# Performance work log

Hardware: AMD Instinct MI355X
Metric: run time of the kernel (lower is better)

The kernel has to match this reference:

```python
import jax, jax.numpy as jnp
import numpy as np

B, NQ, NK, D, H, DFF = 4, 1024, 1024, 1024, 16, 4096
DH = D // H
SCALE = 1.0 / np.sqrt(D).astype(np.float32)  # torch code scales by sqrt(dim_V), not head_dim
LN_EPS = 1e-5


def setup_inputs() -> dict:
    key = jax.random.key(0)
    ks = jax.random.split(key, 20)
    s = lambda fan_in: 1.0 / np.sqrt(fan_in).astype(np.float32)
    inp = {
        "Q": jax.random.normal(ks[0], (B, NQ, D), jnp.float32),
        "K": jax.random.normal(ks[1], (B, NK, D), jnp.float32),
        # attention projections (torch Linear stored here as [in, out])
        "Wq": jax.random.uniform(ks[2], (D, D), jnp.float32, -s(D), s(D)),
        "bq": jnp.zeros((D,), jnp.float32),
        "Wk": jax.random.uniform(ks[3], (D, D), jnp.float32, -s(D), s(D)),
        "bk": jnp.zeros((D,), jnp.float32),
        "Wv": jax.random.uniform(ks[4], (D, D), jnp.float32, -s(D), s(D)),
        "bv": jnp.zeros((D,), jnp.float32),
        "Wo": jax.random.uniform(ks[5], (D, D), jnp.float32, -s(D), s(D)),
        "bo": jnp.zeros((D,), jnp.float32),
        # FFN
        "W1": jax.random.uniform(ks[6], (D, DFF), jnp.float32, -s(D), s(D)),
        "b1": jnp.zeros((DFF,), jnp.float32),
        "W2": jax.random.uniform(ks[7], (DFF, D), jnp.float32, -s(DFF), s(DFF)),
        "b2": jnp.zeros((D,), jnp.float32),
        # LayerNorms
        "g0": jnp.ones((D,), jnp.float32),
        "be0": jnp.zeros((D,), jnp.float32),
        "g1": jnp.ones((D,), jnp.float32),
        "be1": jnp.zeros((D,), jnp.float32),
    }
    return inp


def _layernorm(x, g, b):
    mu = x.mean(-1, keepdims=True)
    var = ((x - mu) ** 2).mean(-1, keepdims=True)
    return (x - mu) * jax.lax.rsqrt(var + LN_EPS) * g + b


def reference(Q, K, Wq, bq, Wk, bk, Wv, bv, Wo, bo, W1, b1, W2, b2, g0, be0, g1, be1):
    # multi-head attention (MHA path, mask=None)
    q = (Q @ Wq + bq).reshape(B, NQ, H, DH)
    k = (K @ Wk + bk).reshape(B, NK, H, DH)
    v = (K @ Wv + bv).reshape(B, NK, H, DH)
    E = jnp.einsum("bqhd,bkhd->bhqk", q, k) * SCALE  # [B,H,NQ,NK]
    A = jax.nn.softmax(E, axis=-1)
    O = jnp.einsum("bhqk,bkhd->bqhd", A, v).reshape(B, NQ, D)
    O = O @ Wo + bo
    # residual + LN0
    X = _layernorm(Q + O, g0, be0)
    # FFN + residual + LN1
    Y = jnp.maximum(X @ W1 + b1, 0.0) @ W2 + b2
    return _layernorm(X + Y, g1, be1)
```

## Files before the change

kernel.cpp:

```cpp
#include <hip/hip_runtime.h>
#include <math.h>

#define B_   4
#define NQ_  1024
#define NK_  1024
#define D_   1024
#define H_   16
#define DH_  64
#define DFF_ 4096
#define SCALE_ (1.0f/32.0f)
#define LN_EPS_ 1e-5f

typedef __attribute__((ext_vector_type(8))) short bf16x8_t;
typedef __attribute__((ext_vector_type(4))) float f32x4_t;

__device__ __forceinline__ ushort f2bf_rne(float x) {
    unsigned u = __float_as_uint(x);
    unsigned r = (u + 0x7FFFu + ((u >> 16) & 1u)) >> 16;
    return (ushort)r;
}
__device__ __forceinline__ float bf2f(ushort h) {
    return __uint_as_float(((unsigned)h) << 16);
}

__device__ __forceinline__ void gl_lds16(const ushort* g, ushort* l) {
    __builtin_amdgcn_global_load_lds(
        (const __attribute__((address_space(1))) unsigned int*)g,
        (__attribute__((address_space(3))) unsigned int*)l, 16, 0, 0);
}

__global__ __launch_bounds__(256) void split_rows(const float* __restrict__ src,
        ushort* __restrict__ hi, ushort* __restrict__ lo, int n4)
{
    int i = blockIdx.x * 256 + threadIdx.x;
    if (i >= n4) return;
    float4 v = ((const float4*)src)[i];
    ushort4 h, l;
    h.x = f2bf_rne(v.x); l.x = f2bf_rne(v.x - bf2f(h.x));
    h.y = f2bf_rne(v.y); l.y = f2bf_rne(v.y - bf2f(h.y));
    h.z = f2bf_rne(v.z); l.z = f2bf_rne(v.z - bf2f(h.z));
    h.w = f2bf_rne(v.w); l.w = f2bf_rne(v.w - bf2f(h.w));
    ((ushort4*)hi)[i] = h;
    ((ushort4*)lo)[i] = l;
}

__global__ __launch_bounds__(256) void split_tr(const float* __restrict__ Wsrc,
        ushort* __restrict__ th, ushort* __restrict__ tl, int K, int N)
{
    __shared__ float tile[32][33];
    const int nb = blockIdx.x * 32, kb = blockIdx.y * 32;
    const int t = threadIdx.x;
    {
        int r = t >> 3, c4 = (t & 7) * 4;
        float4 v = *(const float4*)&Wsrc[(size_t)(kb + r) * N + nb + c4];
        tile[r][c4 + 0] = v.x; tile[r][c4 + 1] = v.y;
        tile[r][c4 + 2] = v.z; tile[r][c4 + 3] = v.w;
    }
    __syncthreads();
    {
        int n = t >> 3, k4 = (t & 7) * 4;
        float a0 = tile[k4 + 0][n], a1 = tile[k4 + 1][n];
        float a2 = tile[k4 + 2][n], a3 = tile[k4 + 3][n];
        ushort4 h, l;
        h.x = f2bf_rne(a0); l.x = f2bf_rne(a0 - bf2f(h.x));
        h.y = f2bf_rne(a1); l.y = f2bf_rne(a1 - bf2f(h.y));
        h.z = f2bf_rne(a2); l.z = f2bf_rne(a2 - bf2f(h.z));
        h.w = f2bf_rne(a3); l.w = f2bf_rne(a3 - bf2f(h.w));
        size_t o = (size_t)(nb + n) * K + kb + k4;
        *(ushort4*)&th[o] = h;
        *(ushort4*)&tl[o] = l;
    }
}

template<bool RELU, int OMODE>
__device__ __forceinline__ void gemm_body(
        const ushort* __restrict__ Ah, const ushort* __restrict__ Al,
        const ushort* __restrict__ Bh, const ushort* __restrict__ Bl,
        const float* __restrict__ bias,
        float* __restrict__ C, ushort* __restrict__ Ch, ushort* __restrict__ Cl,
        int M, int N, int Kd, int Klen, int brow, int bcol)
{
    __shared__ __align__(16) ushort S[2][4][128 * 32];

    const int t    = threadIdx.x;
    const int lane = t & 63;
    const int w    = t >> 6;
    const int wr   = (w >> 1) * 64;
    const int wc   = (w & 1) * 64;
    const int fr   = lane & 15;
    const int g    = lane >> 4;
    const int sS   = ((g ^ ((fr >> 1) & 3)) << 3);
    const int cl   = lane & 15;
    const int rq   = (lane >> 4) * 4;

    float bpre[4];
    #pragma unroll
    for (int j = 0; j < 4; ++j)
        bpre[j] = bias ? bias[bcol + wc + j * 16 + cl] : 0.f;

    f32x4_t acc[4][4];
    #pragma unroll
    for (int i = 0; i < 4; ++i)
        #pragma unroll
        for (int j = 0; j < 4; ++j)
            acc[i][j] = (f32x4_t){0.f, 0.f, 0.f, 0.f};

    const int lrow  = lane >> 2;
    const int lslot = ((lane & 3) ^ ((lane >> 3) & 3)) << 3;
    const int c0    = w * 2;

    auto issue2 = [&](const ushort* gpp, int rb, int pl, int buf, int k0) {
        #pragma unroll
        for (int ii = 0; ii < 2; ++ii) {
            int c = c0 + ii;
            gl_lds16(gpp + (size_t)(rb + c * 16 + lrow) * Kd + k0 + lslot,
                     &S[buf][pl][c * 512]);
        }
    };

    bf16x8_t ahf[4], bhf[4], blf[4], alf[4];

    issue2(Ah, brow, 0, 0, 0);
    issue2(Bh, bcol, 2, 0, 0);
    issue2(Bl, bcol, 3, 0, 0);
    issue2(Al, brow, 1, 0, 0);
    asm volatile("s_waitcnt vmcnt(4)" ::: "memory");
    __builtin_amdgcn_s_barrier();

    const int NT = Klen >> 5;
    for (int tt = 0; tt < NT; ++tt) {
        const int cur = tt & 1, nxt = cur ^ 1;
        const int kn  = (tt + 1) << 5;
        const bool more = (tt + 1 < NT);

        #pragma unroll
        for (int i = 0; i < 4; ++i)
            ahf[i] = *(const bf16x8_t*)&S[cur][0][(wr + i * 16 + fr) * 32 + sS];
        #pragma unroll
        for (int j = 0; j < 4; ++j)
            bhf[j] = *(const bf16x8_t*)&S[cur][2][(wc + j * 16 + fr) * 32 + sS];
        if (more) {
            issue2(Ah, brow, 0, nxt, kn);
            issue2(Bh, bcol, 2, nxt, kn);
            asm volatile("s_waitcnt vmcnt(6)" ::: "memory");
        } else {
            asm volatile("s_waitcnt vmcnt(2)" ::: "memory");
        }
        __builtin_amdgcn_s_barrier();
        asm volatile("s_waitcnt lgkmcnt(0)" ::: "memory");
        __builtin_amdgcn_sched_barrier(0);
        __builtin_amdgcn_s_setprio(1);
        #pragma unroll
        for (int i = 0; i < 4; ++i)
            #pragma unroll
            for (int j = 0; j < 4; ++j)
                acc[i][j] = __builtin_amdgcn_mfma_f32_16x16x32_bf16(ahf[i], bhf[j], acc[i][j], 0, 0, 0);
        __builtin_amdgcn_s_setprio(0);
        __builtin_amdgcn_s_barrier();

        #pragma unroll
        for (int j = 0; j < 4; ++j)
            blf[j] = *(const bf16x8_t*)&S[cur][3][(wc + j * 16 + fr) * 32 + sS];
        if (more) {
            issue2(Bl, bcol, 3, nxt, kn);
            asm volatile("s_waitcnt vmcnt(6)" ::: "memory");
        } else {
            asm volatile("s_waitcnt vmcnt(0)" ::: "memory");
        }
        __builtin_amdgcn_s_barrier();
        asm volatile("s_waitcnt lgkmcnt(0)" ::: "memory");
        __builtin_amdgcn_sched_barrier(0);
        __builtin_amdgcn_s_setprio(1);
        #pragma unroll
        for (int i = 0; i < 4; ++i)
            #pragma unroll
            for (int j = 0; j < 4; ++j)
                acc[i][j] = __builtin_amdgcn_mfma_f32_16x16x32_bf16(ahf[i], blf[j], acc[i][j], 0, 0, 0);
        __builtin_amdgcn_s_setprio(0);
        __builtin_amdgcn_s_barrier();

        #pragma unroll
        for (int i = 0; i < 4; ++i)
            alf[i] = *(const bf16x8_t*)&S[cur][1][(wr + i * 16 + fr) * 32 + sS];
        if (more) {
            issue2(Al, brow, 1, nxt, kn);
            asm volatile("s_waitcnt vmcnt(4)" ::: "memory");
        }
        __builtin_amdgcn_s_barrier();
        asm volatile("s_waitcnt lgkmcnt(0)" ::: "memory");
        __builtin_amdgcn_sched_barrier(0);
        __builtin_amdgcn_s_setprio(1);
        #pragma unroll
        for (int i = 0; i < 4; ++i)
            #pragma unroll
            for (int j = 0; j < 4; ++j)
                acc[i][j] = __builtin_amdgcn_mfma_f32_16x16x32_bf16(alf[i], bhf[j], acc[i][j], 0, 0, 0);
        __builtin_amdgcn_s_setprio(0);
        __builtin_amdgcn_s_barrier();
    }

    if (OMODE == 0) {
        #pragma unroll
        for (int j = 0; j < 4; ++j) {
            int col = bcol + wc + j * 16 + cl;
            #pragma unroll
            for (int i = 0; i < 4; ++i)
                #pragma unroll
                for (int r = 0; r < 4; ++r) {
                    int row = brow + wr + i * 16 + rq + r;
                    float v = acc[i][j][r] + bpre[j];
                    if (RELU) v = fmaxf(v, 0.f);
                    C[(size_t)row * N + col] = v;
                }
        }
    } else {
        float* E = (float*)&S[0][0][0] + w * 4096;
        #pragma unroll
        for (int j = 0; j < 4; ++j) {
            #pragma unroll
            for (int i = 0; i < 4; ++i)
                #pragma unroll
                for (int r = 0; r < 4; ++r) {
                    float v = acc[i][j][r] + bpre[j];
                    if (RELU) v = fmaxf(v, 0.f);
                    E[(i * 16 + rq + r) * 64 + j * 16 + cl] = v;
                }
        }
        __syncthreads();
        const int rr8 = lane >> 3;
        const int c8  = (lane & 7) * 8;
        #pragma unroll
        for (int p = 0; p < 8; ++p) {
            int rl = p * 8 + rr8;
            float4 va = *(float4*)&E[rl * 64 + c8];
            float4 vb = *(float4*)&E[rl * 64 + c8 + 4];
            float v[8] = {va.x, va.y, va.z, va.w, vb.x, vb.y, vb.z, vb.w};
            bf16x8_t hv, lv;
            #pragma unroll
            for (int q = 0; q < 8; ++q) {
                ushort hh = f2bf_rne(v[q]);
                hv[q] = (short)hh;
                lv[q] = (short)f2bf_rne(v[q] - bf2f(hh));
            }
            size_t o = (size_t)(brow + wr + rl) * N + (bcol + wc + c8);
            *(bf16x8_t*)&Ch[o] = hv;
            if (OMODE == 1) *(bf16x8_t*)&Cl[o] = lv;
        }
    }
}

__device__ __forceinline__ void swz_block(int& brow, int& bcol, int tile) {
    const int nx  = gridDim.x;
    const int lin = blockIdx.y * nx + blockIdx.x;
    const int cpx = (nx * gridDim.y) >> 3;
    const int swz = (lin & 7) * cpx + (lin >> 3);
    brow = (swz / nx) * tile;
    bcol = (swz % nx) * tile;
}

template<bool RELU, int OMODE>
__global__ __launch_bounds__(256) void gemm_mfma(
        const ushort* __restrict__ Ah, const ushort* __restrict__ Al,
        const ushort* __restrict__ Bh, const ushort* __restrict__ Bl,
        const float* __restrict__ bias,
        float* __restrict__ C, ushort* __restrict__ Ch, ushort* __restrict__ Cl,
        int M, int N, int Kd)
{
    int brow, bcol;
    swz_block(brow, bcol, 128);
    gemm_body<RELU, OMODE>(Ah, Al, Bh, Bl, bias, C, Ch, Cl, M, N, Kd, Kd, brow, bcol);
}

__global__ __launch_bounds__(256) void gemm_splitk2(
        const ushort* __restrict__ Ah, const ushort* __restrict__ Al,
        const ushort* __restrict__ Bh, const ushort* __restrict__ Bl,
        const float* __restrict__ bias,
        float* __restrict__ C0, float* __restrict__ C1,
        int M, int N, int Kd)
{
    int brow, bcol;
    swz_block(brow, bcol, 128);
    const int z = blockIdx.z;
    const int Kh2 = Kd >> 1;
    const int ko  = z * Kh2;
    gemm_body<false, 0>(Ah + ko, Al + ko, Bh + ko, Bl + ko,
                        z == 0 ? bias : nullptr,
                        z == 0 ? C0 : C1, nullptr, nullptr,
                        M, N, Kd, Kh2, brow, bcol);
}

struct QkvArgs {
    const ushort* Ah[3]; const ushort* Al[3];
    const ushort* Bh[3]; const ushort* Bl[3];
    const float*  bias[3];
    ushort*       Co[3];
};

__global__ __launch_bounds__(256) void gemm_qkv(QkvArgs qa, int M, int N, int Kd)
{
    int brow, bcol;
    swz_block(brow, bcol, 128);
    const int z = blockIdx.z;
    gemm_body<false, 2>(qa.Ah[z], qa.Al[z], qa.Bh[z], qa.Bl[z], qa.bias[z],
                        nullptr, qa.Co[z], nullptr, M, N, Kd, Kd, brow, bcol);
}

__global__ __launch_bounds__(256) void flash_attn_mfma(
        const ushort* __restrict__ qh, const ushort* __restrict__ kh,
        const ushort* __restrict__ vh,
        ushort* __restrict__ Oh, ushort* __restrict__ Ol)
{
    __shared__ __align__(16) ushort SMEM[8192];
    ushort* sk  = SMEM;
    ushort* svt = SMEM + 2304;
    ushort* pw0 = SMEM + 4864;

    const int bid  = blockIdx.x;
    const int slot = bid >> 3;
    const int bh   = (bid & 7) * 8 + (slot >> 4);
    const int qt   = slot & 15;
    const int b    = bh >> 4;
    const int h    = bh & 15;
    const int qb   = qt * 64;

    const int t = threadIdx.x, lane = t & 63, w = t >> 6;
    const int l15 = lane & 15, g = lane >> 4;

    bf16x8_t qf[2];
    {
        size_t qrow = ((size_t)(b * NQ_) + qb + w * 16 + l15) * D_ + h * DH_;
        qf[0] = *(const bf16x8_t*)&qh[qrow + 0  + 8 * g];
        qf[1] = *(const bf16x8_t*)&qh[qrow + 32 + 8 * g];
    }

    f32x4_t acc[4];
    #pragma unroll
    for (int dt = 0; dt < 4; ++dt) acc[dt] = (f32x4_t){0.f, 0.f, 0.f, 0.f};
    float m = -INFINITY, l = 0.0f;

    const int kkv = t >> 3,  kds = (t & 7) * 8;
    const int vkv = t & 31,  vds = (t >> 5) * 8;
    const size_t kvbase = (size_t)(b * NK_) * D_ + h * DH_;

    bf16x8_t kreg = *(const bf16x8_t*)&kh[kvbase + (size_t)kkv * D_ + kds];
    bf16x8_t vreg = *(const bf16x8_t*)&vh[kvbase + (size_t)vkv * D_ + vds];

    ushort* pw = pw0 + w * 640;

    for (int kt = 0; kt < NK_; kt += 32) {
        __syncthreads();
        *(bf16x8_t*)&sk[kkv * 72 + kds] = kreg;
        #pragma unroll
        for (int j = 0; j < 8; ++j)
            svt[(vds + j) * 40 + vkv] = (ushort)vreg[j];
        __syncthreads();
        if (kt + 32 < NK_) {
            kreg = *(const bf16x8_t*)&kh[kvbase + (size_t)(kt + 32 + kkv) * D_ + kds];
            vreg = *(const bf16x8_t*)&vh[kvbase + (size_t)(kt + 32 + vkv) * D_ + vds];
        }

        f32x4_t s0 = (f32x4_t){0.f,0.f,0.f,0.f};
        f32x4_t s1 = (f32x4_t){0.f,0.f,0.f,0.f};
        #pragma unroll
        for (int c = 0; c < 2; ++c) {
            bf16x8_t k0 = *(const bf16x8_t*)&sk[(l15     ) * 72 + 32 * c + 8 * g];
            bf16x8_t k1 = *(const bf16x8_t*)&sk[(l15 + 16) * 72 + 32 * c + 8 * g];
            s0 = __builtin_amdgcn_mfma_f32_16x16x32_bf16(k0, qf[c], s0, 0, 0, 0);
            s1 = __builtin_amdgcn_mfma_f32_16x16x32_bf16(k1, qf[c], s1, 0, 0, 0);
        }

        float e0[4], e1[4];
        #pragma unroll
        for (int r = 0; r < 4; ++r) { e0[r] = s0[r] * SCALE_; e1[r] = s1[r] * SCALE_; }
        float tmax = fmaxf(fmaxf(fmaxf(e0[0], e0[1]), fmaxf(e0[2], e0[3])),
                           fmaxf(fmaxf(e1[0], e1[1]), fmaxf(e1[2], e1[3])));
        tmax = fmaxf(tmax, __shfl_xor(tmax, 16, 64));
        tmax = fmaxf(tmax, __shfl_xor(tmax, 32, 64));
        float mn   = fmaxf(m, tmax);
        float corr = __expf(m - mn);
        float p0[4], p1[4];
        float ps = 0.f;
        #pragma unroll
        for (int r = 0; r < 4; ++r) {
            p0[r] = __expf(e0[r] - mn);
            p1[r] = __expf(e1[r] - mn);
            ps += p0[r] + p1[r];
        }
        ps += __shfl_xor(ps, 16, 64);
        ps += __shfl_xor(ps, 32, 64);
        l = l * corr + ps;
        m = mn;
        #pragma unroll
        for (int dt = 0; dt < 4; ++dt)
            #pragma unroll
            for (int r = 0; r < 4; ++r)
                acc[dt][r] *= corr;

        ushort4 pk0, pk1;
        pk0.x = f2bf_rne(p0[0]); pk0.y = f2bf_rne(p0[1]);
        pk0.z = f2bf_rne(p0[2]); pk0.w = f2bf_rne(p0[3]);
        pk1.x = f2bf_rne(p1[0]); pk1.y = f2bf_rne(p1[1]);
        pk1.z = f2bf_rne(p1[2]); pk1.w = f2bf_rne(p1[3]);
        *(ushort4*)&pw[l15 * 40 + 4 * g]      = pk0;
        *(ushort4*)&pw[l15 * 40 + 16 + 4 * g] = pk1;
        bf16x8_t pa = *(const bf16x8_t*)&pw[l15 * 40 + 8 * g];

        #pragma unroll
        for (int dt = 0; dt < 4; ++dt) {
            bf16x8_t vf = *(const bf16x8_t*)&svt[(16 * dt + l15) * 40 + 8 * g];
            acc[dt] = __builtin_amdgcn_mfma_f32_16x16x32_bf16(vf, pa, acc[dt], 0, 0, 0);
        }
    }

    __syncthreads();
    float invl = 1.0f / l;
    float* Ew = (float*)SMEM + w * 1024;
    #pragma unroll
    for (int dt = 0; dt < 4; ++dt)
        #pragma unroll
        for (int r = 0; r < 4; ++r)
            Ew[(16 * dt + 4 * g + r) * 16 + l15] = acc[dt][r] * invl;
    const int ql = lane >> 2;
    const int dc = (lane & 3) * 16;
    float ov[16];
    #pragma unroll
    for (int j = 0; j < 16; ++j) ov[j] = Ew[(dc + j) * 16 + ql];
    bf16x8_t hv0, hv1, lv0, lv1;
    #pragma unroll
    for (int j = 0; j < 8; ++j) {
        ushort ha = f2bf_rne(ov[j]);
        ushort hb = f2bf_rne(ov[8 + j]);
        hv0[j] = (short)ha; lv0[j] = (short)f2bf_rne(ov[j] - bf2f(ha));
        hv1[j] = (short)hb; lv1[j] = (short)f2bf_rne(ov[8 + j] - bf2f(hb));
    }
    size_t orow = ((size_t)(b * NQ_) + qb + w * 16 + ql) * D_ + h * DH_ + dc;
    *(bf16x8_t*)&Oh[orow]     = hv0;
    *(bf16x8_t*)&Oh[orow + 8] = hv1;
    *(bf16x8_t*)&Ol[orow]     = lv0;
    *(bf16x8_t*)&Ol[orow + 8] = lv1;
}

template<bool SPLIT>
__global__ __launch_bounds__(256) void add_ln3(const float* __restrict__ a0,
        const float* __restrict__ a1, const float* __restrict__ r,
        const float* __restrict__ g, const float* __restrict__ be,
        float* __restrict__ out, ushort* __restrict__ oh, ushort* __restrict__ ol)
{
    const int row = blockIdx.x;
    const int t = threadIdx.x;
    float vals[4];
    float s1 = 0.0f, s2 = 0.0f;
    #pragma unroll
    for (int i = 0; i < 4; ++i) {
        int col = t + i * 256;
        size_t o = (size_t)row * D_ + col;
        float vv = a0[o] + a1[o] + r[o];
        vals[i] = vv;
        s1 += vv;
        s2 += vv * vv;
    }
    #pragma unroll
    for (int off = 32; off > 0; off >>= 1) {
        s1 += __shfl_down(s1, off, 64);
        s2 += __shfl_down(s2, off, 64);
    }
    __shared__ float p1[4], p2[4];
    const int wave = t >> 6;
    if ((t & 63) == 0) { p1[wave] = s1; p2[wave] = s2; }
    __syncthreads();
    s1 = p1[0] + p1[1] + p1[2] + p1[3];
    s2 = p2[0] + p2[1] + p2[2] + p2[3];
    const float mean = s1 * (1.0f / D_);
    const float var  = s2 * (1.0f / D_) - mean * mean;
    const float rstd = rsqrtf(var + LN_EPS_);
    #pragma unroll
    for (int i = 0; i < 4; ++i) {
        int col = t + i * 256;
        float v = (vals[i] - mean) * rstd * g[col] + be[col];
        out[(size_t)row * D_ + col] = v;
        if (SPLIT) {
            ushort h = f2bf_rne(v);
            oh[(size_t)row * D_ + col] = h;
            ol[(size_t)row * D_ + col] = f2bf_rne(v - bf2f(h));
        }
    }
}

extern "C" void kernel_launch(void* const* d_in, const int* in_sizes, int n_in,
                              void* d_out, int out_size, void* d_ws, size_t ws_size,
                              hipStream_t stream)
{
    const float* Q   = (const float*)d_in[0];
    const float* K   = (const float*)d_in[1];
    const float* Wq  = (const float*)d_in[2];
    const float* bq  = (const float*)d_in[3];
    const float* Wk  = (const float*)d_in[4];
    const float* bk  = (const float*)d_in[5];
    const float* Wv  = (const float*)d_in[6];
    const float* bv  = (const float*)d_in[7];
    const float* Wo  = (const float*)d_in[8];
    const float* bo  = (const float*)d_in[9];
    const float* W1  = (const float*)d_in[10];
    const float* b1  = (const float*)d_in[11];
    const float* W2  = (const float*)d_in[12];
    const float* b2  = (const float*)d_in[13];
    const float* g0  = (const float*)d_in[14];
    const float* be0 = (const float*)d_in[15];
    const float* g1  = (const float*)d_in[16];
    const float* be1 = (const float*)d_in[17];

    unsigned char* Wb = (unsigned char*)d_ws;
    const size_t MBy = 1ull << 20;

    ushort* Qh   = (ushort*)(Wb +  0 * MBy);
    ushort* Ql   = (ushort*)(Wb +  8 * MBy);
    ushort* Kh   = (ushort*)(Wb + 16 * MBy);
    ushort* Kl   = (ushort*)(Wb + 24 * MBy);
    ushort* Wqh  = (ushort*)(Wb + 32 * MBy);
    ushort* Wql  = (ushort*)(Wb + 34 * MBy);
    ushort* Wkh  = (ushort*)(Wb + 36 * MBy);
    ushort* Wkl  = (ushort*)(Wb + 38 * MBy);
    ushort* Wvh  = (ushort*)(Wb + 40 * MBy);
    ushort* Wvl  = (ushort*)(Wb + 42 * MBy);
    ushort* Woh  = (ushort*)(Wb + 44 * MBy);
    ushort* Wol  = (ushort*)(Wb + 46 * MBy);
    ushort* qhp  = (ushort*)(Wb + 48 * MBy);
    ushort* khp  = (ushort*)(Wb + 56 * MBy);
    ushort* vhp  = (ushort*)(Wb + 64 * MBy);
    ushort* aOh  = (ushort*)(Wb + 72 * MBy);
    ushort* aOl  = (ushort*)(Wb + 80 * MBy);

    float*  oprj0 = (float*)(Wb + 16 * MBy);
    float*  oprj1 = (float*)(Wb + 56 * MBy);
    float*  Xf    = (float*)(Wb +  0 * MBy);
    ushort* Xh    = (ushort*)(Wb + 32 * MBy);
    ushort* Xl    = (ushort*)(Wb + 40 * MBy);
    ushort* W1h   = (ushort*)(Wb + 16 * MBy);
    ushort* W1l   = (ushort*)(Wb + 24 * MBy);
    ushort* Hih   = (ushort*)(Wb + 80 * MBy);
    ushort* Hil   = (ushort*)(Wb + 48 * MBy);
    ushort* W2h   = (ushort*)(Wb + 16 * MBy);
    ushort* W2l   = (ushort*)(Wb + 24 * MBy);
    float*  Y0    = (float*)(Wb + 32 * MBy);
    float*  Y1    = (float*)d_out;

    const int M = B_ * NQ_;
    const int n4act = M * D_ / 4;
    dim3 blk(256);
    dim3 gQKV(D_ / 128, M / 128, 3);
    dim3 gSK(D_ / 128, M / 128, 2);
    dim3 gF(DFF_ / 128, M / 128);

    split_rows<<<n4act / 256, blk, 0, stream>>>(Q, Qh, Ql, n4act);
    split_rows<<<n4act / 256, blk, 0, stream>>>(K, Kh, Kl, n4act);
    split_tr<<<dim3(D_/32, D_/32), blk, 0, stream>>>(Wq, Wqh, Wql, D_, D_);
    split_tr<<<dim3(D_/32, D_/32), blk, 0, stream>>>(Wk, Wkh, Wkl, D_, D_);
    split_tr<<<dim3(D_/32, D_/32), blk, 0, stream>>>(Wv, Wvh, Wvl, D_, D_);
    split_tr<<<dim3(D_/32, D_/32), blk, 0, stream>>>(Wo, Woh, Wol, D_, D_);

    QkvArgs qa;
    qa.Ah[0] = Qh;  qa.Al[0] = Ql;  qa.Bh[0] = Wqh; qa.Bl[0] = Wql; qa.bias[0] = bq; qa.Co[0] = qhp;
    qa.Ah[1] = Kh;  qa.Al[1] = Kl;  qa.Bh[1] = Wkh; qa.Bl[1] = Wkl; qa.bias[1] = bk; qa.Co[1] = khp;
    qa.Ah[2] = Kh;  qa.Al[2] = Kl;  qa.Bh[2] = Wvh; qa.Bl[2] = Wvl; qa.bias[2] = bv; qa.Co[2] = vhp;
    gemm_qkv<<<gQKV, blk, 0, stream>>>(qa, M, D_, D_);

    flash_attn_mfma<<<dim3(1024), blk, 0, stream>>>(qhp, khp, vhp, aOh, aOl);

    gemm_splitk2<<<gSK, blk, 0, stream>>>(aOh, aOl, Woh, Wol, bo, oprj0, oprj1, M, D_, D_);
    add_ln3<true><<<M, blk, 0, stream>>>(oprj0, oprj1, Q, g0, be0, Xf, Xh, Xl);

    split_tr<<<dim3(DFF_/32, D_/32), blk, 0, stream>>>(W1, W1h, W1l, D_, DFF_);
    gemm_mfma<true,1><<<gF, blk, 0, stream>>>(Xh, Xl, W1h, W1l, b1, nullptr, Hih, Hil, M, DFF_, D_);
    split_tr<<<dim3(D_/32, DFF_/32), blk, 0, stream>>>(W2, W2h, W2l, DFF_, D_);

    gemm_splitk2<<<gSK, blk, 0, stream>>>(Hih, Hil, W2h, W2l, b2, Y0, Y1, M, D_, DFF_);
    add_ln3<false><<<M, blk, 0, stream>>>(Y0, Y1, Xf, g1, be1, (float*)d_out, nullptr, nullptr);
}
```

Baseline: 413.3 us.

## Use 256x256 tile, 512-thread GEMM kernel for FFN1 layer

Adds a dedicated FFN1 GEMM kernel with 256x256 output tiles and 8 waves per block, replacing the 128x128 generic kernel. Each wave computes a 128x64 subtile, with staged loads of the hi/lo bf16 split operands interleaved with the three MFMA passes. The larger tiles raise arithmetic intensity and cut global/L2 traffic per FLOP. In exchange the grid shrinks to 256 blocks, which may underfill the GPU's 256 CUs at one block each, and the larger LDS and register footprint lowers occupancy.

```diff
diff --git a/kernel.cpp b/kernel.cpp
--- a/kernel.cpp
+++ b/kernel.cpp
@@ -72,6 +72,15 @@
     }
 }
 
+__device__ __forceinline__ void swz_block(int& brow, int& bcol, int tile) {
+    const int nx  = gridDim.x;
+    const int lin = blockIdx.y * nx + blockIdx.x;
+    const int cpx = (nx * gridDim.y) >> 3;
+    const int swz = (lin & 7) * cpx + (lin >> 3);
+    brow = (swz / nx) * tile;
+    bcol = (swz % nx) * tile;
+}
+
 template<bool RELU, int OMODE>
 __device__ __forceinline__ void gemm_body(
         const ushort* __restrict__ Ah, const ushort* __restrict__ Al,
@@ -249,15 +258,6 @@
     }
 }
 
-__device__ __forceinline__ void swz_block(int& brow, int& bcol, int tile) {
-    const int nx  = gridDim.x;
-    const int lin = blockIdx.y * nx + blockIdx.x;
-    const int cpx = (nx * gridDim.y) >> 3;
-    const int swz = (lin & 7) * cpx + (lin >> 3);
-    brow = (swz / nx) * tile;
-    bcol = (swz % nx) * tile;
-}
-
 template<bool RELU, int OMODE>
 __global__ __launch_bounds__(256) void gemm_mfma(
         const ushort* __restrict__ Ah, const ushort* __restrict__ Al,
@@ -303,6 +303,170 @@
     const int z = blockIdx.z;
     gemm_body<false, 2>(qa.Ah[z], qa.Al[z], qa.Bh[z], qa.Bl[z], qa.bias[z],
                         nullptr, qa.Co[z], nullptr, M, N, Kd, Kd, brow, bcol);
+}
+
+__global__ __launch_bounds__(512) void gemm_ffn1_256(
+        const ushort* __restrict__ Ah, const ushort* __restrict__ Al,
+        const ushort* __restrict__ Bh, const ushort* __restrict__ Bl,
+        const float* __restrict__ bias,
+        ushort* __restrict__ Ch, ushort* __restrict__ Cl,
+        int M, int N, int Kd)
+{
+    __shared__ __align__(16) ushort S[2][4][256 * 32];
+
+    const int t    = threadIdx.x;
+    const int lane = t & 63;
+    const int w    = t >> 6;
+    const int wr   = (w >> 2) * 128;
+    const int wc   = (w & 3) * 64;
+    const int fr   = lane & 15;
+    const int g    = lane >> 4;
+    const int sS   = ((g ^ ((fr >> 1) & 3)) << 3);
+    const int cl   = lane & 15;
+    const int rq   = (lane >> 4) * 4;
+
+    int brow, bcol;
+    swz_block(brow, bcol, 256);
+
+    float bpre[4];
+    #pragma unroll
+    for (int j = 0; j < 4; ++j) bpre[j] = bias[bcol + wc + j * 16 + cl];
+
+    f32x4_t acc[8][4];
+    #pragma unroll
+    for (int i = 0; i < 8; ++i)
+        #pragma unroll
+        for (int j = 0; j < 4; ++j)
+            acc[i][j] = (f32x4_t){0.f, 0.f, 0.f, 0.f};
+
+    const int lrow  = lane >> 2;
+    const int lslot = ((lane & 3) ^ ((lane >> 3) & 3)) << 3;
+    const int c0    = w * 2;
+
+    auto issue2 = [&](const ushort* gpp, int rb, int pl, int buf, int k0) {
+        #pragma unroll
+        for (int ii = 0; ii < 2; ++ii) {
+            int c = c0 + ii;
+            gl_lds16(gpp + (size_t)(rb + c * 16 + lrow) * Kd + k0 + lslot,
+                     &S[buf][pl][c * 512]);
+        }
+    };
+
+    bf16x8_t ahf[8], bhf[4], blf[4], alf[8];
+
+    issue2(Ah, brow, 0, 0, 0);
+    issue2(Bh, bcol, 2, 0, 0);
+    issue2(Bl, bcol, 3, 0, 0);
+    issue2(Al, brow, 1, 0, 0);
+    asm volatile("s_waitcnt vmcnt(4)" ::: "memory");
+    __builtin_amdgcn_s_barrier();
+
+    const int NT = Kd >> 5;
+    for (int tt = 0; tt < NT; ++tt) {
+        const int cur = tt & 1, nxt = cur ^ 1;
+        const int kn  = (tt + 1) << 5;
+        const bool more = (tt + 1 < NT);
+
+        #pragma unroll
+        for (int i = 0; i < 8; ++i)
+            ahf[i] = *(const bf16x8_t*)&S[cur][0][(wr + i * 16 + fr) * 32 + sS];
+        #pragma unroll
+        for (int j = 0; j < 4; ++j)
+            bhf[j] = *(const bf16x8_t*)&S[cur][2][(wc + j * 16 + fr) * 32 + sS];
+        if (more) {
+            issue2(Ah, brow, 0, nxt, kn);
+            issue2(Bh, bcol, 2, nxt, kn);
+            asm volatile("s_waitcnt vmcnt(6)" ::: "memory");
+        } else {
+            asm volatile("s_waitcnt vmcnt(2)" ::: "memory");
+        }
+        __builtin_amdgcn_s_barrier();
+        asm volatile("s_waitcnt lgkmcnt(0)" ::: "memory");
+        __builtin_amdgcn_sched_barrier(0);
+        __builtin_amdgcn_s_setprio(1);
+        #pragma unroll
+        for (int i = 0; i < 8; ++i)
+            #pragma unroll
+            for (int j = 0; j < 4; ++j)
+                acc[i][j] = __builtin_amdgcn_mfma_f32_16x16x32_bf16(ahf[i], bhf[j], acc[i][j], 0, 0, 0);
+        __builtin_amdgcn_s_setprio(0);
+        __builtin_amdgcn_s_barrier();
+
+        #pragma unroll
+        for (int j = 0; j < 4; ++j)
+            blf[j] = *(const bf16x8_t*)&S[cur][3][(wc + j * 16 + fr) * 32 + sS];
+        if (more) {
+            issue2(Bl, bcol, 3, nxt, kn);
+            asm volatile("s_waitcnt vmcnt(6)" ::: "memory");
+        } else {
+            asm volatile("s_waitcnt vmcnt(0)" ::: "memory");
+        }
+        __builtin_amdgcn_s_barrier();
+        asm volatile("s_waitcnt lgkmcnt(0)" ::: "memory");
+        __builtin_amdgcn_sched_barrier(0);
+        __builtin_amdgcn_s_setprio(1);
+        #pragma unroll
+        for (int i = 0; i < 8; ++i)
+            #pragma unroll
+            for (int j = 0; j < 4; ++j)
+                acc[i][j] = __builtin_amdgcn_mfma_f32_16x16x32_bf16(ahf[i], blf[j], acc[i][j], 0, 0, 0);
+        __builtin_amdgcn_s_setprio(0);
+        __builtin_amdgcn_s_barrier();
+
+        #pragma unroll
+        for (int i = 0; i < 8; ++i)
+            alf[i] = *(const bf16x8_t*)&S[cur][1][(wr + i * 16 + fr) * 32 + sS];
+        if (more) {
+            issue2(Al, brow, 1, nxt, kn);
+            asm volatile("s_waitcnt vmcnt(4)" ::: "memory");
+        }
+        __builtin_amdgcn_s_barrier();
+        asm volatile("s_waitcnt lgkmcnt(0)" ::: "memory");
+        __builtin_amdgcn_sched_barrier(0);
+        __builtin_amdgcn_s_setprio(1);
+        #pragma unroll
+        for (int i = 0; i < 8; ++i)
+            #pragma unroll
+            for (int j = 0; j < 4; ++j)
+                acc[i][j] = __builtin_amdgcn_mfma_f32_16x16x32_bf16(alf[i], bhf[j], acc[i][j], 0, 0, 0);
+        __builtin_amdgcn_s_setprio(0);
+        __builtin_amdgcn_s_barrier();
+    }
+
+    __syncthreads();
+    float* E = (float*)&S[0][0][0] + w * 4096;
+    const int rr8 = lane >> 3;
+    const int c8  = (lane & 7) * 8;
+    #pragma unroll
+    for (int pass = 0; pass < 2; ++pass) {
+        #pragma unroll
+        for (int i = 0; i < 4; ++i) {
+            #pragma unroll
+            for (int j = 0; j < 4; ++j)
+                #pragma unroll
+                for (int r = 0; r < 4; ++r) {
+                    float v = fmaxf(acc[pass * 4 + i][j][r] + bpre[j], 0.f);
+                    E[(i * 16 + rq + r) * 64 + j * 16 + cl] = v;
+                }
+        }
+        #pragma unroll
+        for (int p = 0; p < 8; ++p) {
+            int rl = p * 8 + rr8;
+            float4 va = *(float4*)&E[rl * 64 + c8];
+            float4 vb = *(float4*)&E[rl * 64 + c8 + 4];
+            float v[8] = {va.x, va.y, va.z, va.w, vb.x, vb.y, vb.z, vb.w};
+            bf16x8_t hv, lv;
+            #pragma unroll
+            for (int q = 0; q < 8; ++q) {
+                ushort hh = f2bf_rne(v[q]);
+                hv[q] = (short)hh;
+                lv[q] = (short)f2bf_rne(v[q] - bf2f(hh));
+            }
+            size_t o = (size_t)(brow + wr + pass * 64 + rl) * N + (bcol + wc + c8);
+            *(bf16x8_t*)&Ch[o] = hv;
+            *(bf16x8_t*)&Cl[o] = lv;
+        }
+    }
 }
 
 __global__ __launch_bounds__(256) void flash_attn_mfma(
@@ -549,7 +713,6 @@
     dim3 blk(256);
     dim3 gQKV(D_ / 128, M / 128, 3);
     dim3 gSK(D_ / 128, M / 128, 2);
-    dim3 gF(DFF_ / 128, M / 128);
 
     split_rows<<<n4act / 256, blk, 0, stream>>>(Q, Qh, Ql, n4act);
     split_rows<<<n4act / 256, blk, 0, stream>>>(K, Kh, Kl, n4act);
@@ -570,7 +733,8 @@
     add_ln3<true><<<M, blk, 0, stream>>>(oprj0, oprj1, Q, g0, be0, Xf, Xh, Xl);
 
     split_tr<<<dim3(DFF_/32, D_/32), blk, 0, stream>>>(W1, W1h, W1l, D_, DFF_);
-    gemm_mfma<true,1><<<gF, blk, 0, stream>>>(Xh, Xl, W1h, W1l, b1, nullptr, Hih, Hil, M, DFF_, D_);
+    gemm_ffn1_256<<<dim3(DFF_/256, M/256), dim3(512), 0, stream>>>(
+        Xh, Xl, W1h, W1l, b1, Hih, Hil, M, DFF_, D_);
     split_tr<<<dim3(D_/32, DFF_/32), blk, 0, stream>>>(W2, W2h, W2l, DFF_, D_);
 
     gemm_splitk2<<<gSK, blk, 0, stream>>>(Hih, Hil, W2h, W2l, b2, Y0, Y1, M, D_, DFF_);
```

Measured after the change: 396.9 us. 4.0% less time.
